# Optimization experiments

Hardware: AMD Instinct MI355X
Metric: run time of the kernel (lower is better)

## Reference

```python
import jax, jax.numpy as jnp
import numpy as np

EPS = 1e-5

def _conv1x1_bn(x, W, b, g, beta):
    # 1x1 conv == channel matmul; BN in training mode uses batch stats over (N,H,W)
    y = jnp.einsum('bchw,oc->bohw', x, W) + b[None, :, None, None]
    mu = jnp.mean(y, axis=(0, 2, 3))
    var = jnp.var(y, axis=(0, 2, 3))
    y = (y - mu[None, :, None, None]) * jax.lax.rsqrt(var + EPS)[None, :, None, None]
    return y * g[None, :, None, None] + beta[None, :, None, None]


def setup_inputs() -> dict:
    key = jax.random.key(0)
    ks = jax.random.split(key, 7)
    b, c, h, w = 8, 256, 64, 64
    sc = 1.0 / np.sqrt(c)
    inp = {
        'x': jax.random.normal(ks[0], (b, c, h, w), jnp.float32),
        'Wq': jax.random.normal(ks[1], (c, c), jnp.float32) * sc,
        'bq': jax.random.normal(ks[2], (c,), jnp.float32) * 0.02,
        'gq': jnp.ones((c,), jnp.float32),
        'betaq': jnp.zeros((c,), jnp.float32),
        'Wk': jax.random.normal(ks[3], (c, c), jnp.float32) * sc,
        'bk': jax.random.normal(ks[4], (c,), jnp.float32) * 0.02,
        'gk': jnp.ones((c,), jnp.float32),
        'betak': jnp.zeros((c,), jnp.float32),
        'Wv': jax.random.normal(ks[5], (c, c), jnp.float32) * sc,
        'bv': jax.random.normal(ks[6], (c,), jnp.float32) * 0.02,
        'gv': jnp.ones((c,), jnp.float32),
        'betav': jnp.zeros((c,), jnp.float32),
    }
    return inp


def reference(x, Wq, bq, gq, betaq, Wk, bk, gk, betak, Wv, bv, gv, betav):
    b, c, h, w = x.shape
    scale = float(h) ** (-0.5)
    Q = _conv1x1_bn(x, Wq, bq, gq, betaq).reshape(b, c, h * w)
    K = _conv1x1_bn(x, Wk, bk, gk, betak).reshape(b, c, h * w)
    V = _conv1x1_bn(x, Wv, bv, gv, betav).reshape(b, c, h * w)
    # un-normalized attention (no softmax)
    pixelMap = jnp.einsum('bcq,bck->bqk', Q, K) * scale  # [b, N, N]
    out = jnp.einsum('bqk,bck->bcq', pixelMap, V)        # [b, c, N]
    return out.reshape(b, c, h, w)
```

## Files before the change

kernel.cpp:

```cpp
#include <hip/hip_runtime.h>
#include <hip/hip_bf16.h>


#define BB 8
#define CC 256
#define NPIX 4096
#define PTOT 32768
#define EPSV 1e-5f
#define SCALEV 0.125f

#define OFF_PG    0L
#define OFF_SP    3145728L
#define OFF_S     3162112L
#define OFF_GHAT  3164160L
#define OFF_XBAR  3229696L
#define OFF_WP    3229952L
#define OFF_WKTF  3426560L
#define OFF_WVTF  3492096L
#define OFF_CVEC  3557632L
#define OFF_U     3558400L
#define OFF_W2    3560448L
#define OFF_HB    3562496L
#define OFF_Y     3564544L
#define OFF_R     3564800L
#define OFF_OFFV  3565056L
#define OFF_GBF   3567104L
#define OFF_WQT   3829248L
#define OFF_WKT   3862016L
#define OFF_WVB   3894784L
#define OFF_ZT    3927552L
#define OFF_FT    3960320L
#define OFF_TBF   4222464L

typedef __attribute__((ext_vector_type(8))) short short8;
typedef __attribute__((ext_vector_type(4))) float f32x4;

#define MFMA16(a, b, c) __builtin_amdgcn_mfma_f32_16x16x32_bf16((a), (b), (c), 0, 0, 0)

__device__ __forceinline__ ushort f2bf(float f) {
    union { float f; unsigned u; } v; v.f = f;
    const unsigned r = (v.u + 0x7FFFu + ((v.u >> 16) & 1u)) >> 16;
    return (ushort)r;
}

__device__ __forceinline__ float bf2f(ushort u) {
    union { unsigned u; float f; } v; v.u = ((unsigned)u) << 16;
    return v.f;
}

__device__ __forceinline__ ushort2 f2bf2(float a, float b) {
    __hip_bfloat162 h = __float22bfloat162_rn(float2{a, b});
    union { __hip_bfloat162 h; ushort2 u; } v; v.h = h;
    return v.u;
}

__device__ __forceinline__ float block_reduce(float v, float* red, int tid) {
    red[tid] = v; __syncthreads();
    for (int st = 128; st > 0; st >>= 1) {
        if (tid < st) red[tid] += red[tid + st];
        __syncthreads();
    }
    float r = red[0]; __syncthreads();
    return r;
}

__device__ __forceinline__ float2 wred2(float a, float b, float* red8, int tid) {
    #pragma unroll
    for (int s = 32; s > 0; s >>= 1) {
        a += __shfl_xor(a, s);
        b += __shfl_xor(b, s);
    }
    if ((tid & 63) == 0) { red8[(tid >> 6) * 2] = a; red8[(tid >> 6) * 2 + 1] = b; }
    __syncthreads();
    const float ra = red8[0] + red8[2] + red8[4] + red8[6];
    const float rb = red8[1] + red8[3] + red8[5] + red8[7];
    __syncthreads();
    return float2{ra, rb};
}

__global__ __launch_bounds__(256) void gram_mfma(const float* __restrict__ x,
                                                 float* __restrict__ Pg,
                                                 float* __restrict__ Sp,
                                                 float* __restrict__ Ghat) {
    __shared__ __align__(16) ushort Ab[128 * 72];
    __shared__ __align__(16) ushort Bb[128 * 72];
    __shared__ float rs[128];
    const int tid = threadIdx.x;
    const int ks = blockIdx.x, b = blockIdx.y, tt = blockIdx.z;
    const int lb = (tt * 8 + b) * 8 + ks;
    if (lb < 64) {
        #pragma unroll
        for (int i = 0; i < 4; ++i) Ghat[lb * 1024 + i * 256 + tid] = 0.f;
    }
    const int it = (tt == 1) ? 1 : 0;
    const int jt = (tt == 0) ? 0 : 1;
    const bool diag = (tt < 2);
    const int i0 = it * 128, j0 = jt * 128, k0 = ks * 512;
    const float* xb = x + (long)b * CC * NPIX;
    const int c = tid & 15, rp = tid >> 4;
    const int wave = tid >> 6, lane = tid & 63;
    const int wr = (wave >> 1) * 64, wc = (wave & 1) * 64;
    const int m = lane & 15, q8 = (lane >> 4) * 8;

    if (tid < 128) rs[tid] = 0.f;
    float rloc[8] = {};
    f32x4 acc[4][4];
    #pragma unroll
    for (int a = 0; a < 4; ++a)
        #pragma unroll
        for (int q = 0; q < 4; ++q) acc[a][q] = (f32x4){0.f, 0.f, 0.f, 0.f};

    const float* Abase = xb + (long)i0 * NPIX + k0 + c * 4;
    const float* Bbase = xb + (long)j0 * NPIX + k0 + c * 4;

    float4 va[8], vb[8];
    #pragma unroll
    for (int pp = 0; pp < 8; ++pp)
        va[pp] = *(const float4*)&Abase[(long)(pp * 16 + rp) * NPIX];
    if (!diag) {
        #pragma unroll
        for (int pp = 0; pp < 8; ++pp)
            vb[pp] = *(const float4*)&Bbase[(long)(pp * 16 + rp) * NPIX];
    }

    for (int kc = 0; kc < 512; kc += 64) {
        __syncthreads();
        #pragma unroll
        for (int pp = 0; pp < 8; ++pp) {
            const int row = pp * 16 + rp;
            const float4 v = va[pp];
            rloc[pp] += v.x + v.y + v.z + v.w;
            const ushort2 w01 = f2bf2(v.x, v.y);
            const ushort2 w23 = f2bf2(v.z, v.w);
            ushort4 w; w.x = w01.x; w.y = w01.y; w.z = w23.x; w.w = w23.y;
            *(ushort4*)&Ab[row * 72 + c * 4] = w;
        }
        if (!diag) {
            #pragma unroll
            for (int pp = 0; pp < 8; ++pp) {
                const int row = pp * 16 + rp;
                const float4 v = vb[pp];
                const ushort2 w01 = f2bf2(v.x, v.y);
                const ushort2 w23 = f2bf2(v.z, v.w);
                ushort4 w; w.x = w01.x; w.y = w01.y; w.z = w23.x; w.w = w23.y;
                *(ushort4*)&Bb[row * 72 + c * 4] = w;
            }
        }
        const int kn = kc + 64;
        if (kn < 512) {
            #pragma unroll
            for (int pp = 0; pp < 8; ++pp)
                va[pp] = *(const float4*)&Abase[(long)(pp * 16 + rp) * NPIX + kn];
            if (!diag) {
                #pragma unroll
                for (int pp = 0; pp < 8; ++pp)
                    vb[pp] = *(const float4*)&Bbase[(long)(pp * 16 + rp) * NPIX + kn];
            }
        }
        __syncthreads();
        const ushort* Bsrc = diag ? Ab : Bb;
        #pragma unroll
        for (int kk = 0; kk < 2; ++kk) {
            short8 af[4], bfv[4];
            #pragma unroll
            for (int a = 0; a < 4; ++a)
                af[a] = *(const short8*)&Ab[(wr + a * 16 + m) * 72 + kk * 32 + q8];
            #pragma unroll
            for (int q = 0; q < 4; ++q)
                bfv[q] = *(const short8*)&Bsrc[(wc + q * 16 + m) * 72 + kk * 32 + q8];
            #pragma unroll
            for (int a = 0; a < 4; ++a)
                #pragma unroll
                for (int q = 0; q < 4; ++q)
                    acc[a][q] = MFMA16(af[a], bfv[q], acc[a][q]);
        }
    }
    if (diag) {
        #pragma unroll
        for (int pp = 0; pp < 8; ++pp) atomicAdd(&rs[pp * 16 + rp], rloc[pp]);
        __syncthreads();
        if (tid < 128) Sp[(((long)ks * 8 + b) * 2 + it) * 128 + tid] = rs[tid];
    }
    float* Pt = Pg + (((long)ks * 8 + b) * 3 + tt) * 16384;
    const int rq = (lane >> 4) * 4;
    #pragma unroll
    for (int a = 0; a < 4; ++a) {
        #pragma unroll
        for (int q = 0; q < 4; ++q) {
            const int col = wc + q * 16 + m;
            #pragma unroll
            for (int reg = 0; reg < 4; ++reg)
                Pt[(long)(wr + a * 16 + rq + reg) * 128 + col] = acc[a][q][reg];
        }
    }
}

__global__ __launch_bounds__(256) void reduce_mirror(const float* __restrict__ Pg,
                                                     const float* __restrict__ Sp,
                                                     ushort* __restrict__ Gbf,
                                                     float* __restrict__ Ghat,
                                                     float* __restrict__ S,
                                                     float* __restrict__ xbar) {
    const int blk = blockIdx.x, tid = threadIdx.x;
    if (blk == 384) {
        const int it2 = tid >> 7, rr = tid & 127;
        float xacc = 0.f;
        for (int b = 0; b < BB; ++b) {
            float acc = 0.f;
            #pragma unroll
            for (int ks = 0; ks < 8; ++ks)
                acc += Sp[(((long)ks * 8 + b) * 2 + it2) * 128 + rr];
            S[b * 256 + tid] = acc;
            xacc += acc;
        }
        xbar[tid] = xacc * (1.0f / PTOT);
        return;
    }
    __shared__ float tile[32][33];
    const int tt = blk >> 7;
    const int sub = (blk >> 3) & 15;
    const int b = blk & 7;
    const int sr = (sub >> 2) * 32, sc = (sub & 3) * 32;
    const int it = (tt == 1) ? 1 : 0;
    const int jt = (tt == 0) ? 0 : 1;
    const bool offd = (tt == 2);
    const int gi0 = it * 128 + sr, gj0 = jt * 128 + sc;
    const int r = tid >> 3, c4 = (tid & 7) * 4;
    const float inv = 1.0f / PTOT;

    float s0 = 0.f, s1 = 0.f, s2 = 0.f, s3 = 0.f;
    #pragma unroll
    for (int ks = 0; ks < 8; ++ks) {
        const float4 v = *(const float4*)&Pg[(((long)ks * 8 + b) * 3 + tt) * 16384
                                             + (long)(sr + r) * 128 + sc + c4];
        s0 += v.x; s1 += v.y; s2 += v.z; s3 += v.w;
    }
    ushort4 w;
    w.x = f2bf(s0); w.y = f2bf(s1); w.z = f2bf(s2); w.w = f2bf(s3);
    *(ushort4*)&Gbf[(long)b * 65536 + (long)(gi0 + r) * 256 + gj0 + c4] = w;
    float* gd = &Ghat[(long)(gi0 + r) * 256 + gj0 + c4];
    atomicAdd(gd + 0, s0 * inv);
    atomicAdd(gd + 1, s1 * inv);
    atomicAdd(gd + 2, s2 * inv);
    atomicAdd(gd + 3, s3 * inv);
    if (offd) {
        tile[r][c4 + 0] = s0; tile[r][c4 + 1] = s1;
        tile[r][c4 + 2] = s2; tile[r][c4 + 3] = s3;
        __syncthreads();
        const float t0 = tile[c4 + 0][r], t1 = tile[c4 + 1][r];
        const float t2 = tile[c4 + 2][r], t3 = tile[c4 + 3][r];
        ushort4 tw;
        tw.x = f2bf(t0); tw.y = f2bf(t1); tw.z = f2bf(t2); tw.w = f2bf(t3);
        *(ushort4*)&Gbf[(long)b * 65536 + (long)(gj0 + r) * 256 + gi0 + c4] = tw;
        float* gm = &Ghat[(long)(gj0 + r) * 256 + gi0 + c4];
        atomicAdd(gm + 0, t0 * inv);
        atomicAdd(gm + 1, t1 * inv);
        atomicAdd(gm + 2, t2 * inv);
        atomicAdd(gm + 3, t3 * inv);
    }
}

__global__ __launch_bounds__(256) void stats_quad(const float* __restrict__ Wq, const float* __restrict__ Wk,
                           const float* __restrict__ Wv, const float* __restrict__ Ghat,
                           const float* __restrict__ xbar,
                           const float* bq, const float* gq, const float* betaq,
                           const float* bk, const float* gk, const float* betak,
                           const float* bv, const float* gv, const float* betav,
                           float* __restrict__ Wp, float* __restrict__ cvec,
                           ushort* __restrict__ WqT, ushort* __restrict__ WkT,
                           ushort* __restrict__ Wvb, float* __restrict__ WkTf,
                           float* __restrict__ WvTf) {
    const int og = blockIdx.x, t = blockIdx.y, tid = threadIdx.x;
    const int o0 = og * 4;
    const float* Wt  = t == 0 ? Wq : (t == 1 ? Wk : Wv);
    const float* bt  = t == 0 ? bq : (t == 1 ? bk : bv);
    const float* gt  = t == 0 ? gq : (t == 1 ? gk : gv);
    const float* bet = t == 0 ? betaq : (t == 1 ? betak : betav);
    __shared__ float wrows[4][256];
    __shared__ float red8[8];
    #pragma unroll
    for (int i = 0; i < 4; ++i) wrows[i][tid] = Wt[(o0 + i) * 256 + tid];
    const float xb = xbar[tid];
    __syncthreads();
    const float* grow = Ghat + (long)tid * 256;
    float tj[4] = {0.f, 0.f, 0.f, 0.f};
    #pragma unroll 8
    for (int k = 0; k < 256; k += 4) {
        const float4 g = *(const float4*)&grow[k];
        #pragma unroll
        for (int i = 0; i < 4; ++i)
            tj[i] += g.x * wrows[i][k]     + g.y * wrows[i][k + 1]
                   + g.z * wrows[i][k + 2] + g.w * wrows[i][k + 3];
    }
    #pragma unroll
    for (int i = 0; i < 4; ++i) {
        const int o = o0 + i;
        const float wv = wrows[i][tid];
        const float2 qw = wred2(wv * tj[i], wv * xb, red8, tid);
        const float bo = bt[o];
        const float mu = qw.y + bo;
        const float var = qw.x + 2.f * bo * mu - bo * bo - mu * mu;
        const float a = gt[o] * rsqrtf(var + EPSV);
        const float wpv = a * wv;
        Wp[(long)t * 65536 + o * 256 + tid] = wpv;
        const ushort wb = f2bf(wpv);
        if (t == 0) {
            WqT[(long)tid * 256 + o] = wb;
        } else if (t == 1) {
            WkT[(long)tid * 256 + o] = wb;
            WkTf[(long)tid * 256 + o] = wpv;
        } else {
            Wvb[(long)o * 256 + tid] = wb;
            WvTf[(long)tid * 256 + o] = wpv;
        }
        if (tid == 0) cvec[t * 256 + o] = a * (bo - mu) + bet[o];
    }
}

__device__ __forceinline__ void gemm_tile(const ushort* __restrict__ Ab,
                                          const ushort* __restrict__ Bb,
                                          ushort* __restrict__ Db,
                                          int m0, int n0, int mode, int bz,
                                          const float* __restrict__ u,
                                          const float* __restrict__ cvec,
                                          const float* __restrict__ r,
                                          const float* __restrict__ hb, int tid) {
    const int wave = tid >> 6, lane = tid & 63;
    const int wr = (wave >> 1) * 64, wc = (wave & 1) * 64;
    const int m = lane & 15, q8 = (lane >> 4) * 8;
    f32x4 acc[4][4];
    #pragma unroll
    for (int a = 0; a < 4; ++a)
        #pragma unroll
        for (int q = 0; q < 4; ++q) acc[a][q] = (f32x4){0.f, 0.f, 0.f, 0.f};
    #pragma unroll
    for (int kk = 0; kk < 8; ++kk) {
        short8 af[4], bfv[4];
        #pragma unroll
        for (int a = 0; a < 4; ++a)
            af[a] = *(const short8*)&Ab[(long)(m0 + wr + a * 16 + m) * 256 + kk * 32 + q8];
        #pragma unroll
        for (int q = 0; q < 4; ++q)
            bfv[q] = *(const short8*)&Bb[(long)(n0 + wc + q * 16 + m) * 256 + kk * 32 + q8];
        #pragma unroll
        for (int a = 0; a < 4; ++a)
            #pragma unroll
            for (int q = 0; q < 4; ++q)
                acc[a][q] = MFMA16(af[a], bfv[q], acc[a][q]);
    }
    const int rq = (lane >> 4) * 4;
    #pragma unroll
    for (int a = 0; a < 4; ++a) {
        #pragma unroll
        for (int q = 0; q < 4; ++q) {
            const int col = n0 + wc + q * 16 + m;
            #pragma unroll
            for (int reg = 0; reg < 4; ++reg) {
                const int row = m0 + wr + a * 16 + rq + reg;
                const float v = acc[a][q][reg];
                if (mode == 0) {
                    Db[(long)col * 256 + row] = f2bf(v);
                } else {
                    const float rv = r[col];
                    const float t2 = hb[bz * 256 + col] + 4096.0f * rv;
                    const float val = SCALEV * (v + u[bz * 256 + row] * rv + cvec[512 + row] * t2);
                    Db[(long)row * 256 + col] = f2bf(val);
                }
            }
        }
    }
}

__global__ __launch_bounds__(256) void zmida(const ushort* __restrict__ WkT,
                                             const ushort* __restrict__ WqT,
                                             ushort* __restrict__ ZT,
                                             const float* __restrict__ Wp,
                                             const float* __restrict__ WkTf,
                                             const float* __restrict__ WvTf,
                                             const float* __restrict__ S,
                                             const float* __restrict__ cvec,
                                             float* __restrict__ u, float* __restrict__ w,
                                             float* __restrict__ y, float* __restrict__ r) {
    const int blk = blockIdx.x, tid = threadIdx.x;
    if (blk < 4) {
        gemm_tile(WkT, WqT, ZT, (blk >> 1) * 128, (blk & 1) * 128, 0, 0,
                  nullptr, nullptr, nullptr, nullptr, tid);
        return;
    }
    const int bidx = blk - 4;
    if (bidx < 8) {
        __shared__ float sh[256];
        sh[tid] = S[bidx * 256 + tid]; __syncthreads();
        float uu = 0.f, ww = 0.f;
        #pragma unroll 8
        for (int j = 0; j < 256; ++j) {
            uu += WvTf[(long)j * 256 + tid] * sh[j];
            ww += WkTf[(long)j * 256 + tid] * sh[j];
        }
        u[bidx * 256 + tid] = uu;
        w[bidx * 256 + tid] = ww;
    } else {
        __shared__ float cqs[256], cks[256];
        cqs[tid] = cvec[tid]; cks[tid] = cvec[256 + tid]; __syncthreads();
        float yy = 0.f, rr = 0.f;
        #pragma unroll 8
        for (int o = 0; o < 256; ++o) {
            yy += Wp[65536L + (long)o * 256 + tid] * cqs[o];
            rr += Wp[(long)o * 256 + tid] * cks[o];
        }
        y[tid] = yy;
        r[tid] = rr;
    }
}

__global__ __launch_bounds__(256) void bcF(const float* __restrict__ Wp,
                                           const ushort* __restrict__ Gbf,
                                           const float* __restrict__ WvTf,
                                           const float* __restrict__ w,
                                           const float* __restrict__ y,
                                           const float* __restrict__ u,
                                           const float* __restrict__ cvec,
                                           float* __restrict__ hb,
                                           float* __restrict__ offv,
                                           const ushort* __restrict__ ZT,
                                           ushort* __restrict__ FT) {
    const int blk = blockIdx.x, tid = threadIdx.x;
    if (blk >= 8) {
        const int idx = blk - 8;
        const int bz = idx >> 2, t = idx & 3;
        gemm_tile(Gbf + (long)bz * 65536, ZT, FT + (long)bz * 65536,
                  (t >> 1) * 128, (t & 1) * 128, 0, 0,
                  nullptr, nullptr, nullptr, nullptr, tid);
        return;
    }
    const int b = blk;
    __shared__ float wl[256], yl[256], gyl[256], red[256], cqs[256], cks[256];
    wl[tid] = w[b * 256 + tid];
    yl[tid] = y[tid];
    cqs[tid] = cvec[tid];
    cks[tid] = cvec[256 + tid];
    const float cv = cvec[512 + tid];
    const float uu = u[b * 256 + tid];
    __syncthreads();
    float hh = 0.f, gg = 0.f;
    #pragma unroll 8
    for (int o = 0; o < 256; ++o) {
        hh += Wp[(long)o * 256 + tid] * wl[o];
        gg += bf2f(Gbf[(long)b * 65536 + (long)o * 256 + tid]) * yl[o];
    }
    hb[b * 256 + tid] = hh;
    gyl[tid] = gg;
    __syncthreads();
    float vg = 0.f;
    #pragma unroll 8
    for (int j = 0; j < 256; ++j) vg += WvTf[(long)j * 256 + tid] * gyl[j];
    const float dkq = block_reduce(cqs[tid] * cks[tid], red, tid);
    const float dwq = block_reduce(wl[tid] * cqs[tid], red, tid);
    offv[b * 256 + tid] = SCALEV * (vg + uu * dkq + cv * (dwq + 4096.0f * dkq));
}

__global__ __launch_bounds__(256) void gemm_T(const ushort* __restrict__ Wvb,
                                              const ushort* __restrict__ FT,
                                              ushort* __restrict__ Tbf,
                                              const float* __restrict__ u,
                                              const float* __restrict__ cvec,
                                              const float* __restrict__ r,
                                              const float* __restrict__ hb) {
    const int bz = blockIdx.z;
    gemm_tile(Wvb, FT + (long)bz * 65536, Tbf + (long)bz * 65536,
              blockIdx.y * 128, blockIdx.x * 128, 1, bz, u, cvec, r, hb, threadIdx.x);
}

__global__ __launch_bounds__(256) void out_mfma(const ushort* __restrict__ Tbf,
                                                const float* __restrict__ x,
                                                const float* __restrict__ offv,
                                                float* __restrict__ out) {
    __shared__ __align__(16) ushort Bs[64 * 264];
    const int tid = threadIdx.x;
    const int p0 = blockIdx.x * 64;
    const int b = blockIdx.y;
    const float* xb = x + (long)b * CC * NPIX;
    const ushort* Tb = Tbf + (long)b * 65536;

    const int c = tid & 15, kq = tid >> 4;
    #pragma unroll
    for (int kt = 0; kt < 4; ++kt) {
        const int k4 = kt * 64 + kq * 4;
        const int p = c * 4;
        const float4 v0 = *(const float4*)&xb[(long)(k4 + 0) * NPIX + p0 + p];
        const float4 v1 = *(const float4*)&xb[(long)(k4 + 1) * NPIX + p0 + p];
        const float4 v2 = *(const float4*)&xb[(long)(k4 + 2) * NPIX + p0 + p];
        const float4 v3 = *(const float4*)&xb[(long)(k4 + 3) * NPIX + p0 + p];
        ushort2 a01, a23;
        ushort4 w;
        a01 = f2bf2(v0.x, v1.x); a23 = f2bf2(v2.x, v3.x);
        w.x = a01.x; w.y = a01.y; w.z = a23.x; w.w = a23.y;
        *(ushort4*)&Bs[(p + 0) * 264 + k4] = w;
        a01 = f2bf2(v0.y, v1.y); a23 = f2bf2(v2.y, v3.y);
        w.x = a01.x; w.y = a01.y; w.z = a23.x; w.w = a23.y;
        *(ushort4*)&Bs[(p + 1) * 264 + k4] = w;
        a01 = f2bf2(v0.z, v1.z); a23 = f2bf2(v2.z, v3.z);
        w.x = a01.x; w.y = a01.y; w.z = a23.x; w.w = a23.y;
        *(ushort4*)&Bs[(p + 2) * 264 + k4] = w;
        a01 = f2bf2(v0.w, v1.w); a23 = f2bf2(v2.w, v3.w);
        w.x = a01.x; w.y = a01.y; w.z = a23.x; w.w = a23.y;
        *(ushort4*)&Bs[(p + 3) * 264 + k4] = w;
    }
    __syncthreads();

    const int wave = tid >> 6, lane = tid & 63;
    const int wr = wave * 64;
    const int m = lane & 15, q8 = (lane >> 4) * 8;
    f32x4 acc[4][4];
    #pragma unroll
    for (int a = 0; a < 4; ++a)
        #pragma unroll
        for (int q = 0; q < 4; ++q) acc[a][q] = (f32x4){0.f, 0.f, 0.f, 0.f};

    #pragma unroll
    for (int kk = 0; kk < 8; ++kk) {
        short8 af[4], bfv[4];
        #pragma unroll
        for (int a = 0; a < 4; ++a)
            af[a] = *(const short8*)&Tb[(long)(wr + a * 16 + m) * 256 + kk * 32 + q8];
        #pragma unroll
        for (int q = 0; q < 4; ++q)
            bfv[q] = *(const short8*)&Bs[(q * 16 + m) * 264 + kk * 32 + q8];
        #pragma unroll
        for (int a = 0; a < 4; ++a)
            #pragma unroll
            for (int q = 0; q < 4; ++q)
                acc[a][q] = MFMA16(af[a], bfv[q], acc[a][q]);
    }

    const int rq = (lane >> 4) * 4;
    #pragma unroll
    for (int a = 0; a < 4; ++a) {
        #pragma unroll
        for (int reg = 0; reg < 4; ++reg) {
            const int row = wr + a * 16 + rq + reg;
            const float off_ = offv[b * CC + row];
            float* orow = &out[((long)b * CC + row) * NPIX + p0];
            #pragma unroll
            for (int q = 0; q < 4; ++q)
                orow[q * 16 + m] = acc[a][q][reg] + off_;
        }
    }
}

extern "C" void kernel_launch(void* const* d_in, const int* in_sizes, int n_in,
                              void* d_out, int out_size, void* d_ws, size_t ws_size,
                              hipStream_t stream) {
    const float* x     = (const float*)d_in[0];
    const float* Wq    = (const float*)d_in[1];
    const float* bq    = (const float*)d_in[2];
    const float* gq    = (const float*)d_in[3];
    const float* betaq = (const float*)d_in[4];
    const float* Wk    = (const float*)d_in[5];
    const float* bk    = (const float*)d_in[6];
    const float* gk    = (const float*)d_in[7];
    const float* betak = (const float*)d_in[8];
    const float* Wv    = (const float*)d_in[9];
    const float* bv    = (const float*)d_in[10];
    const float* gv    = (const float*)d_in[11];
    const float* betav = (const float*)d_in[12];
    float* ws = (float*)d_ws;

    float*  Pg   = ws + OFF_PG;
    float*  Sp   = ws + OFF_SP;
    float*  S    = ws + OFF_S;
    float*  Ghat = ws + OFF_GHAT;
    float*  Xbar = ws + OFF_XBAR;
    float*  Wp   = ws + OFF_WP;
    float*  WkTf = ws + OFF_WKTF;
    float*  WvTf = ws + OFF_WVTF;
    float*  cvec = ws + OFF_CVEC;
    float*  U    = ws + OFF_U;
    float*  W2   = ws + OFF_W2;
    float*  Hb   = ws + OFF_HB;
    float*  Y    = ws + OFF_Y;
    float*  R    = ws + OFF_R;
    float*  OffV = ws + OFF_OFFV;
    ushort* Gbf  = (ushort*)(ws + OFF_GBF);
    ushort* WqT  = (ushort*)(ws + OFF_WQT);
    ushort* WkT  = (ushort*)(ws + OFF_WKT);
    ushort* Wvb  = (ushort*)(ws + OFF_WVB);
    ushort* ZT   = (ushort*)(ws + OFF_ZT);
    ushort* FT   = (ushort*)(ws + OFF_FT);
    ushort* Tbf  = (ushort*)(ws + OFF_TBF);

    gram_mfma<<<dim3(8, 8, 3), 256, 0, stream>>>(x, Pg, Sp, Ghat);
    reduce_mirror<<<385, 256, 0, stream>>>(Pg, Sp, Gbf, Ghat, S, Xbar);
    stats_quad<<<dim3(64, 3), 256, 0, stream>>>(Wq, Wk, Wv, Ghat, Xbar,
                                                bq, gq, betaq, bk, gk, betak,
                                                bv, gv, betav, Wp, cvec,
                                                WqT, WkT, Wvb, WkTf, WvTf);
    zmida<<<13, 256, 0, stream>>>(WkT, WqT, ZT, Wp, WkTf, WvTf, S, cvec, U, W2, Y, R);
    bcF<<<40, 256, 0, stream>>>(Wp, Gbf, WvTf, W2, Y, U, cvec, Hb, OffV, ZT, FT);
    gemm_T<<<dim3(2, 2, 8), 256, 0, stream>>>(Wvb, FT, Tbf, U, cvec, R, Hb);
    out_mfma<<<dim3(64, 8), 256, 0, stream>>>(Tbf, x, OffV, (float*)d_out);
}
```

Measured before the change: 197.7 us.

## Fuse all stages into one persistent kernel with global grid barriers

Replaces the seven-kernel launch chain with one persistent 256-block kernel. The stages are separated by an atomic-counter grid barrier, and a union of shared-memory layouts lets each stage reuse the same LDS. This is meant to remove per-launch overhead and the idle tail between small dependent kernels. The intermediate ZT/FT buffers are dropped, and the middle GEMM stages appear to be restructured to keep intermediate tiles in swizzled LDS. The barrier assumes all 256 blocks are co-resident, and its spin has a bounded timeout that could silently break ordering if that assumption fails. It also adds a memset per call.

```diff
diff --git a/kernel.cpp b/kernel.cpp
--- a/kernel.cpp
+++ b/kernel.cpp
@@ -19,18 +19,15 @@
 #define OFF_WVTF  3492096L
 #define OFF_CVEC  3557632L
 #define OFF_U     3558400L
-#define OFF_W2    3560448L
 #define OFF_HB    3562496L
-#define OFF_Y     3564544L
 #define OFF_R     3564800L
 #define OFF_OFFV  3565056L
 #define OFF_GBF   3567104L
 #define OFF_WQT   3829248L
 #define OFF_WKT   3862016L
 #define OFF_WVB   3894784L
-#define OFF_ZT    3927552L
-#define OFF_FT    3960320L
 #define OFF_TBF   4222464L
+#define OFF_CNT   4484608L
 
 typedef __attribute__((ext_vector_type(8))) short short8;
 typedef __attribute__((ext_vector_type(4))) float f32x4;
@@ -78,472 +75,465 @@
     return float2{ra, rb};
 }
 
-__global__ __launch_bounds__(256) void gram_mfma(const float* __restrict__ x,
-                                                 float* __restrict__ Pg,
-                                                 float* __restrict__ Sp,
-                                                 float* __restrict__ Ghat) {
-    __shared__ __align__(16) ushort Ab[128 * 72];
-    __shared__ __align__(16) ushort Bb[128 * 72];
-    __shared__ float rs[128];
-    const int tid = threadIdx.x;
-    const int ks = blockIdx.x, b = blockIdx.y, tt = blockIdx.z;
-    const int lb = (tt * 8 + b) * 8 + ks;
-    if (lb < 64) {
-        #pragma unroll
-        for (int i = 0; i < 4; ++i) Ghat[lb * 1024 + i * 256 + tid] = 0.f;
-    }
-    const int it = (tt == 1) ? 1 : 0;
-    const int jt = (tt == 0) ? 0 : 1;
-    const bool diag = (tt < 2);
-    const int i0 = it * 128, j0 = jt * 128, k0 = ks * 512;
-    const float* xb = x + (long)b * CC * NPIX;
-    const int c = tid & 15, rp = tid >> 4;
-    const int wave = tid >> 6, lane = tid & 63;
-    const int wr = (wave >> 1) * 64, wc = (wave & 1) * 64;
-    const int m = lane & 15, q8 = (lane >> 4) * 8;
-
-    if (tid < 128) rs[tid] = 0.f;
-    float rloc[8] = {};
-    f32x4 acc[4][4];
+__device__ __forceinline__ void gbar(unsigned* cnt, unsigned target) {
+    __syncthreads();
+    if (threadIdx.x == 0) {
+        __threadfence();
+        atomicAdd(cnt, 1u);
+        unsigned spins = 0;
+        while (atomicAdd(cnt, 0u) < target && ++spins < (1u << 18))
+            __builtin_amdgcn_s_sleep(32);
+        __threadfence();
+    }
+    __syncthreads();
+}
+
+union SmemU {
+    struct { ushort Ab[128 * 72]; ushort Bb[128 * 72]; float rs[128]; } g;
+    struct { float tile[32][33]; } rm;
+    struct { float wr4[4][256]; float red8[8]; } st;
+    struct { float sh[256], wl[256], yl[256], gyl[256],
+                   red[256], cqs[256], cks[256]; } vx;
+    struct { ushort zt[64 * 256]; ushort ft[64 * 256]; } ch;
+    struct { ushort Bs[64 * 264]; } op;
+};
+
+__device__ __forceinline__ void mm256x64(f32x4 acc[4][4],
+                                         const ushort* __restrict__ Aglob,
+                                         const ushort* __restrict__ Bglob,
+                                         const ushort* Blds,
+                                         int wave, int m, int qq) {
+    const int q8 = qq * 8;
+    #pragma unroll
+    for (int kk = 0; kk < 8; ++kk) {
+        short8 af[4], bv[4];
+        #pragma unroll
+        for (int a = 0; a < 4; ++a)
+            af[a] = *(const short8*)&Aglob[(long)(wave * 64 + a * 16 + m) * 256 + kk * 32 + q8];
+        #pragma unroll
+        for (int q = 0; q < 4; ++q) {
+            const int col = q * 16 + m;
+            if (Blds) bv[q] = *(const short8*)&Blds[col * 256 + ((kk * 32 + q8) ^ ((col & 7) << 3))];
+            else      bv[q] = *(const short8*)&Bglob[(long)col * 256 + kk * 32 + q8];
+        }
+        #pragma unroll
+        for (int a = 0; a < 4; ++a)
+            #pragma unroll
+            for (int q = 0; q < 4; ++q)
+                acc[a][q] = MFMA16(af[a], bv[q], acc[a][q]);
+    }
+}
+
+__device__ __forceinline__ void st_lds(ushort* L, f32x4 acc[4][4],
+                                       int wave, int m, int qq) {
     #pragma unroll
     for (int a = 0; a < 4; ++a)
         #pragma unroll
-        for (int q = 0; q < 4; ++q) acc[a][q] = (f32x4){0.f, 0.f, 0.f, 0.f};
-
-    const float* Abase = xb + (long)i0 * NPIX + k0 + c * 4;
-    const float* Bbase = xb + (long)j0 * NPIX + k0 + c * 4;
-
-    float4 va[8], vb[8];
-    #pragma unroll
-    for (int pp = 0; pp < 8; ++pp)
-        va[pp] = *(const float4*)&Abase[(long)(pp * 16 + rp) * NPIX];
-    if (!diag) {
+        for (int q = 0; q < 4; ++q) {
+            const int col = q * 16 + m;
+            const int rowb = wave * 64 + a * 16 + qq * 4;
+            const ushort2 p01 = f2bf2(acc[a][q][0], acc[a][q][1]);
+            const ushort2 p23 = f2bf2(acc[a][q][2], acc[a][q][3]);
+            ushort4 w4; w4.x = p01.x; w4.y = p01.y; w4.z = p23.x; w4.w = p23.y;
+            *(ushort4*)&L[col * 256 + (rowb ^ ((col & 7) << 3))] = w4;
+        }
+}
+
+__global__ __launch_bounds__(256, 2) void mono(
+        const float* __restrict__ x,
+        const float* __restrict__ Wq, const float* __restrict__ bq,
+        const float* __restrict__ gq, const float* __restrict__ betaq,
+        const float* __restrict__ Wk, const float* __restrict__ bk,
+        const float* __restrict__ gk, const float* __restrict__ betak,
+        const float* __restrict__ Wv, const float* __restrict__ bv,
+        const float* __restrict__ gv, const float* __restrict__ betav,
+        float* __restrict__ out,
+        float* __restrict__ Pg, float* __restrict__ Sp, float* __restrict__ S,
+        float* __restrict__ Ghat, float* __restrict__ xbar,
+        float* __restrict__ Wp, float* __restrict__ WkTf, float* __restrict__ WvTf,
+        float* __restrict__ cvec, float* __restrict__ u, float* __restrict__ hb,
+        float* __restrict__ r_, float* __restrict__ offv,
+        ushort* __restrict__ Gbf, ushort* __restrict__ WqT, ushort* __restrict__ WkT,
+        ushort* __restrict__ Wvb, ushort* __restrict__ Tbf,
+        unsigned* __restrict__ cnt) {
+    __shared__ SmemU sm;
+    const int blk = blockIdx.x, tid = threadIdx.x;
+    const unsigned NB = gridDim.x;
+
+    if (blk < 64) {
+        #pragma unroll
+        for (int i = 0; i < 4; ++i) Ghat[blk * 1024 + i * 256 + tid] = 0.f;
+    }
+    if (blk < 192) {
+        const int ks = blk & 7, b = (blk >> 3) & 7, tt = blk >> 6;
+        const int it = (tt == 1) ? 1 : 0;
+        const int jt = (tt == 0) ? 0 : 1;
+        const bool diag = (tt < 2);
+        const int i0 = it * 128, j0 = jt * 128, k0 = ks * 512;
+        const float* xb = x + (long)b * CC * NPIX;
+        const int c = tid & 15, rp = tid >> 4;
+        const int wave = tid >> 6, lane = tid & 63;
+        const int wr = (wave >> 1) * 64, wc = (wave & 1) * 64;
+        const int m = lane & 15, q8 = (lane >> 4) * 8;
+
+        if (tid < 128) sm.g.rs[tid] = 0.f;
+        float rloc[8] = {};
+        f32x4 acc[4][4];
+        #pragma unroll
+        for (int a = 0; a < 4; ++a)
+            #pragma unroll
+            for (int q = 0; q < 4; ++q) acc[a][q] = (f32x4){0.f, 0.f, 0.f, 0.f};
+
+        const float* Abase = xb + (long)i0 * NPIX + k0 + c * 4;
+        const float* Bbase = xb + (long)j0 * NPIX + k0 + c * 4;
+
+        float4 va[8], vb[8];
         #pragma unroll
         for (int pp = 0; pp < 8; ++pp)
-            vb[pp] = *(const float4*)&Bbase[(long)(pp * 16 + rp) * NPIX];
-    }
-
-    for (int kc = 0; kc < 512; kc += 64) {
-        __syncthreads();
-        #pragma unroll
-        for (int pp = 0; pp < 8; ++pp) {
-            const int row = pp * 16 + rp;
-            const float4 v = va[pp];
-            rloc[pp] += v.x + v.y + v.z + v.w;
-            const ushort2 w01 = f2bf2(v.x, v.y);
-            const ushort2 w23 = f2bf2(v.z, v.w);
-            ushort4 w; w.x = w01.x; w.y = w01.y; w.z = w23.x; w.w = w23.y;
-            *(ushort4*)&Ab[row * 72 + c * 4] = w;
-        }
+            va[pp] = *(const float4*)&Abase[(long)(pp * 16 + rp) * NPIX];
         if (!diag) {
+            #pragma unroll
+            for (int pp = 0; pp < 8; ++pp)
+                vb[pp] = *(const float4*)&Bbase[(long)(pp * 16 + rp) * NPIX];
+        }
+
+        for (int kc = 0; kc < 512; kc += 64) {
+            __syncthreads();
             #pragma unroll
             for (int pp = 0; pp < 8; ++pp) {
                 const int row = pp * 16 + rp;
-                const float4 v = vb[pp];
+                const float4 v = va[pp];
+                rloc[pp] += v.x + v.y + v.z + v.w;
                 const ushort2 w01 = f2bf2(v.x, v.y);
                 const ushort2 w23 = f2bf2(v.z, v.w);
                 ushort4 w; w.x = w01.x; w.y = w01.y; w.z = w23.x; w.w = w23.y;
-                *(ushort4*)&Bb[row * 72 + c * 4] = w;
-            }
-        }
-        const int kn = kc + 64;
-        if (kn < 512) {
-            #pragma unroll
-            for (int pp = 0; pp < 8; ++pp)
-                va[pp] = *(const float4*)&Abase[(long)(pp * 16 + rp) * NPIX + kn];
+                *(ushort4*)&sm.g.Ab[row * 72 + c * 4] = w;
+            }
             if (!diag) {
                 #pragma unroll
+                for (int pp = 0; pp < 8; ++pp) {
+                    const int row = pp * 16 + rp;
+                    const float4 v = vb[pp];
+                    const ushort2 w01 = f2bf2(v.x, v.y);
+                    const ushort2 w23 = f2bf2(v.z, v.w);
+                    ushort4 w; w.x = w01.x; w.y = w01.y; w.z = w23.x; w.w = w23.y;
+                    *(ushort4*)&sm.g.Bb[row * 72 + c * 4] = w;
+                }
+            }
+            const int kn = kc + 64;
+            if (kn < 512) {
+                #pragma unroll
                 for (int pp = 0; pp < 8; ++pp)
-                    vb[pp] = *(const float4*)&Bbase[(long)(pp * 16 + rp) * NPIX + kn];
-            }
-        }
-        __syncthreads();
-        const ushort* Bsrc = diag ? Ab : Bb;
-        #pragma unroll
-        for (int kk = 0; kk < 2; ++kk) {
+                    va[pp] = *(const float4*)&Abase[(long)(pp * 16 + rp) * NPIX + kn];
+                if (!diag) {
+                    #pragma unroll
+                    for (int pp = 0; pp < 8; ++pp)
+                        vb[pp] = *(const float4*)&Bbase[(long)(pp * 16 + rp) * NPIX + kn];
+                }
+            }
+            __syncthreads();
+            const ushort* Bsrc = diag ? sm.g.Ab : sm.g.Bb;
+            #pragma unroll
+            for (int kk = 0; kk < 2; ++kk) {
+                short8 af[4], bfv[4];
+                #pragma unroll
+                for (int a = 0; a < 4; ++a)
+                    af[a] = *(const short8*)&sm.g.Ab[(wr + a * 16 + m) * 72 + kk * 32 + q8];
+                #pragma unroll
+                for (int q = 0; q < 4; ++q)
+                    bfv[q] = *(const short8*)&Bsrc[(wc + q * 16 + m) * 72 + kk * 32 + q8];
+                #pragma unroll
+                for (int a = 0; a < 4; ++a)
+                    #pragma unroll
+                    for (int q = 0; q < 4; ++q)
+                        acc[a][q] = MFMA16(af[a], bfv[q], acc[a][q]);
+            }
+        }
+        if (diag) {
+            #pragma unroll
+            for (int pp = 0; pp < 8; ++pp) atomicAdd(&sm.g.rs[pp * 16 + rp], rloc[pp]);
+            __syncthreads();
+            if (tid < 128) Sp[(((long)ks * 8 + b) * 2 + it) * 128 + tid] = sm.g.rs[tid];
+        }
+        float* Pt = Pg + (((long)ks * 8 + b) * 3 + tt) * 16384;
+        const int rq = (lane >> 4) * 4;
+        #pragma unroll
+        for (int a = 0; a < 4; ++a) {
+            #pragma unroll
+            for (int q = 0; q < 4; ++q) {
+                const int col = wc + q * 16 + m;
+                #pragma unroll
+                for (int reg = 0; reg < 4; ++reg)
+                    Pt[(long)(wr + a * 16 + rq + reg) * 128 + col] = acc[a][q][reg];
+            }
+        }
+    }
+    gbar(cnt, NB * 1);
+
+    for (int v = blk; v <= 384; v += 256) {
+        if (v == 384) {
+            const int it2 = tid >> 7, rr = tid & 127;
+            float xacc = 0.f;
+            for (int b = 0; b < BB; ++b) {
+                float acc = 0.f;
+                #pragma unroll
+                for (int ks = 0; ks < 8; ++ks)
+                    acc += Sp[(((long)ks * 8 + b) * 2 + it2) * 128 + rr];
+                S[b * 256 + tid] = acc;
+                xacc += acc;
+            }
+            xbar[tid] = xacc * (1.0f / PTOT);
+            continue;
+        }
+        const int tt = v >> 7;
+        const int sub = (v >> 3) & 15;
+        const int b = v & 7;
+        const int sr = (sub >> 2) * 32, sc = (sub & 3) * 32;
+        const int it = (tt == 1) ? 1 : 0;
+        const int jt = (tt == 0) ? 0 : 1;
+        const bool offd = (tt == 2);
+        const int gi0 = it * 128 + sr, gj0 = jt * 128 + sc;
+        const int r = tid >> 3, c4 = (tid & 7) * 4;
+        const float inv = 1.0f / PTOT;
+
+        float s0 = 0.f, s1 = 0.f, s2 = 0.f, s3 = 0.f;
+        #pragma unroll
+        for (int ks = 0; ks < 8; ++ks) {
+            const float4 pv = *(const float4*)&Pg[(((long)ks * 8 + b) * 3 + tt) * 16384
+                                                  + (long)(sr + r) * 128 + sc + c4];
+            s0 += pv.x; s1 += pv.y; s2 += pv.z; s3 += pv.w;
+        }
+        ushort4 w;
+        w.x = f2bf(s0); w.y = f2bf(s1); w.z = f2bf(s2); w.w = f2bf(s3);
+        *(ushort4*)&Gbf[(long)b * 65536 + (long)(gi0 + r) * 256 + gj0 + c4] = w;
+        float* gd = &Ghat[(long)(gi0 + r) * 256 + gj0 + c4];
+        atomicAdd(gd + 0, s0 * inv);
+        atomicAdd(gd + 1, s1 * inv);
+        atomicAdd(gd + 2, s2 * inv);
+        atomicAdd(gd + 3, s3 * inv);
+        if (offd) {
+            sm.rm.tile[r][c4 + 0] = s0; sm.rm.tile[r][c4 + 1] = s1;
+            sm.rm.tile[r][c4 + 2] = s2; sm.rm.tile[r][c4 + 3] = s3;
+            __syncthreads();
+            const float t0 = sm.rm.tile[c4 + 0][r], t1 = sm.rm.tile[c4 + 1][r];
+            const float t2 = sm.rm.tile[c4 + 2][r], t3 = sm.rm.tile[c4 + 3][r];
+            ushort4 tw;
+            tw.x = f2bf(t0); tw.y = f2bf(t1); tw.z = f2bf(t2); tw.w = f2bf(t3);
+            *(ushort4*)&Gbf[(long)b * 65536 + (long)(gj0 + r) * 256 + gi0 + c4] = tw;
+            float* gm = &Ghat[(long)(gj0 + r) * 256 + gi0 + c4];
+            atomicAdd(gm + 0, t0 * inv);
+            atomicAdd(gm + 1, t1 * inv);
+            atomicAdd(gm + 2, t2 * inv);
+            atomicAdd(gm + 3, t3 * inv);
+            __syncthreads();
+        }
+    }
+    gbar(cnt, NB * 2);
+
+    if (blk < 192) {
+        const int og = blk & 63, t = blk >> 6;
+        const int o0 = og * 4;
+        const float* Wt  = t == 0 ? Wq : (t == 1 ? Wk : Wv);
+        const float* bt  = t == 0 ? bq : (t == 1 ? bk : bv);
+        const float* gt  = t == 0 ? gq : (t == 1 ? gk : gv);
+        const float* bet = t == 0 ? betaq : (t == 1 ? betak : betav);
+        #pragma unroll
+        for (int i = 0; i < 4; ++i) sm.st.wr4[i][tid] = Wt[(o0 + i) * 256 + tid];
+        const float xb = xbar[tid];
+        __syncthreads();
+        const float* grow = Ghat + (long)tid * 256;
+        float tj[4] = {0.f, 0.f, 0.f, 0.f};
+        #pragma unroll 8
+        for (int k = 0; k < 256; k += 4) {
+            const float4 g = *(const float4*)&grow[k];
+            #pragma unroll
+            for (int i = 0; i < 4; ++i)
+                tj[i] += g.x * sm.st.wr4[i][k]     + g.y * sm.st.wr4[i][k + 1]
+                       + g.z * sm.st.wr4[i][k + 2] + g.w * sm.st.wr4[i][k + 3];
+        }
+        #pragma unroll
+        for (int i = 0; i < 4; ++i) {
+            const int o = o0 + i;
+            const float wv = sm.st.wr4[i][tid];
+            const float2 qw = wred2(wv * tj[i], wv * xb, sm.st.red8, tid);
+            const float bo = bt[o];
+            const float mu = qw.y + bo;
+            const float var = qw.x + 2.f * bo * mu - bo * bo - mu * mu;
+            const float a = gt[o] * rsqrtf(var + EPSV);
+            const float wpv = a * wv;
+            Wp[(long)t * 65536 + o * 256 + tid] = wpv;
+            const ushort wb = f2bf(wpv);
+            if (t == 0) {
+                WqT[(long)tid * 256 + o] = wb;
+            } else if (t == 1) {
+                WkT[(long)tid * 256 + o] = wb;
+                WkTf[(long)tid * 256 + o] = wpv;
+            } else {
+                Wvb[(long)o * 256 + tid] = wb;
+                WvTf[(long)tid * 256 + o] = wpv;
+            }
+            if (tid == 0) cvec[t * 256 + o] = a * (bo - mu) + bet[o];
+        }
+    }
+    gbar(cnt, NB * 3);
+
+    if (blk < 8) {
+        const int b = blk;
+        sm.vx.sh[tid]  = S[b * 256 + tid];
+        sm.vx.cqs[tid] = cvec[tid];
+        sm.vx.cks[tid] = cvec[256 + tid];
+        __syncthreads();
+        float yy = 0.f, rr = 0.f, uu = 0.f, ww = 0.f;
+        #pragma unroll 8
+        for (int o = 0; o < 256; ++o) {
+            yy += Wp[65536L + (long)o * 256 + tid] * sm.vx.cqs[o];
+            rr += Wp[(long)o * 256 + tid] * sm.vx.cks[o];
+        }
+        #pragma unroll 8
+        for (int j = 0; j < 256; ++j) {
+            uu += WvTf[(long)j * 256 + tid] * sm.vx.sh[j];
+            ww += WkTf[(long)j * 256 + tid] * sm.vx.sh[j];
+        }
+        sm.vx.yl[tid] = yy; sm.vx.wl[tid] = ww;
+        __syncthreads();
+        float hh = 0.f, gg = 0.f;
+        #pragma unroll 8
+        for (int o = 0; o < 256; ++o) {
+            hh += Wp[(long)o * 256 + tid] * sm.vx.wl[o];
+            gg += bf2f(Gbf[(long)b * 65536 + (long)o * 256 + tid]) * sm.vx.yl[o];
+        }
+        hb[b * 256 + tid] = hh;
+        u[b * 256 + tid] = uu;
+        if (blk == 0) r_[tid] = rr;
+        sm.vx.gyl[tid] = gg;
+        __syncthreads();
+        float vg = 0.f;
+        #pragma unroll 8
+        for (int j = 0; j < 256; ++j) vg += WvTf[(long)j * 256 + tid] * sm.vx.gyl[j];
+        const float cv = cvec[512 + tid];
+        const float dkq = block_reduce(sm.vx.cqs[tid] * sm.vx.cks[tid], sm.vx.red, tid);
+        const float dwq = block_reduce(sm.vx.wl[tid] * sm.vx.cqs[tid], sm.vx.red, tid);
+        offv[b * 256 + tid] = SCALEV * (vg + uu * dkq + cv * (dwq + 4096.0f * dkq));
+    }
+    gbar(cnt, NB * 4);
+
+    if (blk < 32) {
+        const int b = blk >> 2, j0 = (blk & 3) * 64;
+        const int wave = tid >> 6, lane = tid & 63;
+        const int m = lane & 15, qq = lane >> 4;
+        f32x4 acc[4][4];
+
+        #pragma unroll
+        for (int a = 0; a < 4; ++a)
+            #pragma unroll
+            for (int q = 0; q < 4; ++q) acc[a][q] = (f32x4){0.f, 0.f, 0.f, 0.f};
+        mm256x64(acc, WkT, WqT + (long)j0 * 256, nullptr, wave, m, qq);
+        st_lds(sm.ch.zt, acc, wave, m, qq);
+        __syncthreads();
+
+        #pragma unroll
+        for (int a = 0; a < 4; ++a)
+            #pragma unroll
+            for (int q = 0; q < 4; ++q) acc[a][q] = (f32x4){0.f, 0.f, 0.f, 0.f};
+        mm256x64(acc, Gbf + (long)b * 65536, nullptr, sm.ch.zt, wave, m, qq);
+        st_lds(sm.ch.ft, acc, wave, m, qq);
+        __syncthreads();
+
+        #pragma unroll
+        for (int a = 0; a < 4; ++a)
+            #pragma unroll
+            for (int q = 0; q < 4; ++q) acc[a][q] = (f32x4){0.f, 0.f, 0.f, 0.f};
+        mm256x64(acc, Wvb, nullptr, sm.ch.ft, wave, m, qq);
+        const int rq4 = qq * 4;
+        #pragma unroll
+        for (int a = 0; a < 4; ++a) {
+            #pragma unroll
+            for (int q = 0; q < 4; ++q) {
+                const int cg = j0 + q * 16 + m;
+                const float rv = r_[cg];
+                const float t2 = hb[b * 256 + cg] + 4096.0f * rv;
+                #pragma unroll
+                for (int reg = 0; reg < 4; ++reg) {
+                    const int row = wave * 64 + a * 16 + rq4 + reg;
+                    const float val = SCALEV * (acc[a][q][reg] + u[b * 256 + row] * rv
+                                                + cvec[512 + row] * t2);
+                    Tbf[(long)b * 65536 + (long)row * 256 + cg] = f2bf(val);
+                }
+            }
+        }
+    }
+    gbar(cnt, NB * 5);
+
+    for (int v = blk; v < 512; v += 256) {
+        const int p0 = (v & 63) * 64;
+        const int b = v >> 6;
+        const float* xb = x + (long)b * CC * NPIX;
+        const ushort* Tb = Tbf + (long)b * 65536;
+        __syncthreads();
+
+        const int c = tid & 15, kq = tid >> 4;
+        #pragma unroll
+        for (int kt = 0; kt < 4; ++kt) {
+            const int k4 = kt * 64 + kq * 4;
+            const int p = c * 4;
+            const float4 v0 = *(const float4*)&xb[(long)(k4 + 0) * NPIX + p0 + p];
+            const float4 v1 = *(const float4*)&xb[(long)(k4 + 1) * NPIX + p0 + p];
+            const float4 v2 = *(const float4*)&xb[(long)(k4 + 2) * NPIX + p0 + p];
+            const float4 v3 = *(const float4*)&xb[(long)(k4 + 3) * NPIX + p0 + p];
+            ushort2 a01, a23;
+            ushort4 w;
+            a01 = f2bf2(v0.x, v1.x); a23 = f2bf2(v2.x, v3.x);
+            w.x = a01.x; w.y = a01.y; w.z = a23.x; w.w = a23.y;
+            *(ushort4*)&sm.op.Bs[(p + 0) * 264 + k4] = w;
+            a01 = f2bf2(v0.y, v1.y); a23 = f2bf2(v2.y, v3.y);
+            w.x = a01.x; w.y = a01.y; w.z = a23.x; w.w = a23.y;
+            *(ushort4*)&sm.op.Bs[(p + 1) * 264 + k4] = w;
+            a01 = f2bf2(v0.z, v1.z); a23 = f2bf2(v2.z, v3.z);
+            w.x = a01.x; w.y = a01.y; w.z = a23.x; w.w = a23.y;
+            *(ushort4*)&sm.op.Bs[(p + 2) * 264 + k4] = w;
+            a01 = f2bf2(v0.w, v1.w); a23 = f2bf2(v2.w, v3.w);
+            w.x = a01.x; w.y = a01.y; w.z = a23.x; w.w = a23.y;
+            *(ushort4*)&sm.op.Bs[(p + 3) * 264 + k4] = w;
+        }
+        __syncthreads();
+
+        const int wave = tid >> 6, lane = tid & 63;
+        const int wr = wave * 64;
+        const int m = lane & 15, q8 = (lane >> 4) * 8;
+        f32x4 acc[4][4];
+        #pragma unroll
+        for (int a = 0; a < 4; ++a)
+            #pragma unroll
+            for (int q = 0; q < 4; ++q) acc[a][q] = (f32x4){0.f, 0.f, 0.f, 0.f};
+
+        #pragma unroll
+        for (int kk = 0; kk < 8; ++kk) {
             short8 af[4], bfv[4];
             #pragma unroll
             for (int a = 0; a < 4; ++a)
-                af[a] = *(const short8*)&Ab[(wr + a * 16 + m) * 72 + kk * 32 + q8];
+                af[a] = *(const short8*)&Tb[(long)(wr + a * 16 + m) * 256 + kk * 32 + q8];
             #pragma unroll
             for (int q = 0; q < 4; ++q)
-                bfv[q] = *(const short8*)&Bsrc[(wc + q * 16 + m) * 72 + kk * 32 + q8];
+                bfv[q] = *(const short8*)&sm.op.Bs[(q * 16 + m) * 264 + kk * 32 + q8];
             #pragma unroll
             for (int a = 0; a < 4; ++a)
                 #pragma unroll
                 for (int q = 0; q < 4; ++q)
                     acc[a][q] = MFMA16(af[a], bfv[q], acc[a][q]);
         }
-    }
-    if (diag) {
-        #pragma unroll
-        for (int pp = 0; pp < 8; ++pp) atomicAdd(&rs[pp * 16 + rp], rloc[pp]);
-        __syncthreads();
-        if (tid < 128) Sp[(((long)ks * 8 + b) * 2 + it) * 128 + tid] = rs[tid];
-    }
-    float* Pt = Pg + (((long)ks * 8 + b) * 3 + tt) * 16384;
-    const int rq = (lane >> 4) * 4;
-    #pragma unroll
-    for (int a = 0; a < 4; ++a) {
-        #pragma unroll
-        for (int q = 0; q < 4; ++q) {
-            const int col = wc + q * 16 + m;
-            #pragma unroll
-            for (int reg = 0; reg < 4; ++reg)
-                Pt[(long)(wr + a * 16 + rq + reg) * 128 + col] = acc[a][q][reg];
-        }
-    }
-}
-
-__global__ __launch_bounds__(256) void reduce_mirror(const float* __restrict__ Pg,
-                                                     const float* __restrict__ Sp,
-                                                     ushort* __restrict__ Gbf,
-                                                     float* __restrict__ Ghat,
-                                                     float* __restrict__ S,
-                                                     float* __restrict__ xbar) {
-    const int blk = blockIdx.x, tid = threadIdx.x;
-    if (blk == 384) {
-        const int it2 = tid >> 7, rr = tid & 127;
-        float xacc = 0.f;
-        for (int b = 0; b < BB; ++b) {
-            float acc = 0.f;
-            #pragma unroll
-            for (int ks = 0; ks < 8; ++ks)
-                acc += Sp[(((long)ks * 8 + b) * 2 + it2) * 128 + rr];
-            S[b * 256 + tid] = acc;
-            xacc += acc;
-        }
-        xbar[tid] = xacc * (1.0f / PTOT);
-        return;
-    }
-    __shared__ float tile[32][33];
-    const int tt = blk >> 7;
-    const int sub = (blk >> 3) & 15;
-    const int b = blk & 7;
-    const int sr = (sub >> 2) * 32, sc = (sub & 3) * 32;
-    const int it = (tt == 1) ? 1 : 0;
-    const int jt = (tt == 0) ? 0 : 1;
-    const bool offd = (tt == 2);
-    const int gi0 = it * 128 + sr, gj0 = jt * 128 + sc;
-    const int r = tid >> 3, c4 = (tid & 7) * 4;
-    const float inv = 1.0f / PTOT;
-
-    float s0 = 0.f, s1 = 0.f, s2 = 0.f, s3 = 0.f;
-    #pragma unroll
-    for (int ks = 0; ks < 8; ++ks) {
-        const float4 v = *(const float4*)&Pg[(((long)ks * 8 + b) * 3 + tt) * 16384
-                                             + (long)(sr + r) * 128 + sc + c4];
-        s0 += v.x; s1 += v.y; s2 += v.z; s3 += v.w;
-    }
-    ushort4 w;
-    w.x = f2bf(s0); w.y = f2bf(s1); w.z = f2bf(s2); w.w = f2bf(s3);
-    *(ushort4*)&Gbf[(long)b * 65536 + (long)(gi0 + r) * 256 + gj0 + c4] = w;
-    float* gd = &Ghat[(long)(gi0 + r) * 256 + gj0 + c4];
-    atomicAdd(gd + 0, s0 * inv);
-    atomicAdd(gd + 1, s1 * inv);
-    atomicAdd(gd + 2, s2 * inv);
-    atomicAdd(gd + 3, s3 * inv);
-    if (offd) {
-        tile[r][c4 + 0] = s0; tile[r][c4 + 1] = s1;
-        tile[r][c4 + 2] = s2; tile[r][c4 + 3] = s3;
-        __syncthreads();
-        const float t0 = tile[c4 + 0][r], t1 = tile[c4 + 1][r];
-        const float t2 = tile[c4 + 2][r], t3 = tile[c4 + 3][r];
-        ushort4 tw;
-        tw.x = f2bf(t0); tw.y = f2bf(t1); tw.z = f2bf(t2); tw.w = f2bf(t3);
-        *(ushort4*)&Gbf[(long)b * 65536 + (long)(gj0 + r) * 256 + gi0 + c4] = tw;
-        float* gm = &Ghat[(long)(gj0 + r) * 256 + gi0 + c4];
-        atomicAdd(gm + 0, t0 * inv);
-        atomicAdd(gm + 1, t1 * inv);
-        atomicAdd(gm + 2, t2 * inv);
-        atomicAdd(gm + 3, t3 * inv);
-    }
-}
-
-__global__ __launch_bounds__(256) void stats_quad(const float* __restrict__ Wq, const float* __restrict__ Wk,
-                           const float* __restrict__ Wv, const float* __restrict__ Ghat,
-                           const float* __restrict__ xbar,
-                           const float* bq, const float* gq, const float* betaq,
-                           const float* bk, const float* gk, const float* betak,
-                           const float* bv, const float* gv, const float* betav,
-                           float* __restrict__ Wp, float* __restrict__ cvec,
-                           ushort* __restrict__ WqT, ushort* __restrict__ WkT,
-                           ushort* __restrict__ Wvb, float* __restrict__ WkTf,
-                           float* __restrict__ WvTf) {
-    const int og = blockIdx.x, t = blockIdx.y, tid = threadIdx.x;
-    const int o0 = og * 4;
-    const float* Wt  = t == 0 ? Wq : (t == 1 ? Wk : Wv);
-    const float* bt  = t == 0 ? bq : (t == 1 ? bk : bv);
-    const float* gt  = t == 0 ? gq : (t == 1 ? gk : gv);
-    const float* bet = t == 0 ? betaq : (t == 1 ? betak : betav);
-    __shared__ float wrows[4][256];
-    __shared__ float red8[8];
-    #pragma unroll
-    for (int i = 0; i < 4; ++i) wrows[i][tid] = Wt[(o0 + i) * 256 + tid];
-    const float xb = xbar[tid];
-    __syncthreads();
-    const float* grow = Ghat + (long)tid * 256;
-    float tj[4] = {0.f, 0.f, 0.f, 0.f};
-    #pragma unroll 8
-    for (int k = 0; k < 256; k += 4) {
-        const float4 g = *(const float4*)&grow[k];
-        #pragma unroll
-        for (int i = 0; i < 4; ++i)
-            tj[i] += g.x * wrows[i][k]     + g.y * wrows[i][k + 1]
-                   + g.z * wrows[i][k + 2] + g.w * wrows[i][k + 3];
-    }
-    #pragma unroll
-    for (int i = 0; i < 4; ++i) {
-        const int o = o0 + i;
-        const float wv = wrows[i][tid];
-        const float2 qw = wred2(wv * tj[i], wv * xb, red8, tid);
-        const float bo = bt[o];
-        const float mu = qw.y + bo;
-        const float var = qw.x + 2.f * bo * mu - bo * bo - mu * mu;
-        const float a = gt[o] * rsqrtf(var + EPSV);
-        const float wpv = a * wv;
-        Wp[(long)t * 65536 + o * 256 + tid] = wpv;
-        const ushort wb = f2bf(wpv);
-        if (t == 0) {
-            WqT[(long)tid * 256 + o] = wb;
-        } else if (t == 1) {
-            WkT[(long)tid * 256 + o] = wb;
-            WkTf[(long)tid * 256 + o] = wpv;
-        } else {
-            Wvb[(long)o * 256 + tid] = wb;
-            WvTf[(long)tid * 256 + o] = wpv;
-        }
-        if (tid == 0) cvec[t * 256 + o] = a * (bo - mu) + bet[o];
-    }
-}
-
-__device__ __forceinline__ void gemm_tile(const ushort* __restrict__ Ab,
-                                          const ushort* __restrict__ Bb,
-                                          ushort* __restrict__ Db,
-                                          int m0, int n0, int mode, int bz,
-                                          const float* __restrict__ u,
-                                          const float* __restrict__ cvec,
-                                          const float* __restrict__ r,
-                                          const float* __restrict__ hb, int tid) {
-    const int wave = tid >> 6, lane = tid & 63;
-    const int wr = (wave >> 1) * 64, wc = (wave & 1) * 64;
-    const int m = lane & 15, q8 = (lane >> 4) * 8;
-    f32x4 acc[4][4];
-    #pragma unroll
-    for (int a = 0; a < 4; ++a)
-        #pragma unroll
-        for (int q = 0; q < 4; ++q) acc[a][q] = (f32x4){0.f, 0.f, 0.f, 0.f};
-    #pragma unroll
-    for (int kk = 0; kk < 8; ++kk) {
-        short8 af[4], bfv[4];
-        #pragma unroll
-        for (int a = 0; a < 4; ++a)
-            af[a] = *(const short8*)&Ab[(long)(m0 + wr + a * 16 + m) * 256 + kk * 32 + q8];
-        #pragma unroll
-        for (int q = 0; q < 4; ++q)
-            bfv[q] = *(const short8*)&Bb[(long)(n0 + wc + q * 16 + m) * 256 + kk * 32 + q8];
-        #pragma unroll
-        for (int a = 0; a < 4; ++a)
-            #pragma unroll
-            for (int q = 0; q < 4; ++q)
-                acc[a][q] = MFMA16(af[a], bfv[q], acc[a][q]);
-    }
-    const int rq = (lane >> 4) * 4;
-    #pragma unroll
-    for (int a = 0; a < 4; ++a) {
-        #pragma unroll
-        for (int q = 0; q < 4; ++q) {
-            const int col = n0 + wc + q * 16 + m;
+
+        const int rq = (lane >> 4) * 4;
+        #pragma unroll
+        for (int a = 0; a < 4; ++a) {
             #pragma unroll
             for (int reg = 0; reg < 4; ++reg) {
-                const int row = m0 + wr + a * 16 + rq + reg;
-                const float v = acc[a][q][reg];
-                if (mode == 0) {
-                    Db[(long)col * 256 + row] = f2bf(v);
-                } else {
-                    const float rv = r[col];
-                    const float t2 = hb[bz * 256 + col] + 4096.0f * rv;
-                    const float val = SCALEV * (v + u[bz * 256 + row] * rv + cvec[512 + row] * t2);
-                    Db[(long)row * 256 + col] = f2bf(val);
-                }
-            }
-        }
-    }
-}
-
-__global__ __launch_bounds__(256) void zmida(const ushort* __restrict__ WkT,
-                                             const ushort* __restrict__ WqT,
-                                             ushort* __restrict__ ZT,
-                                             const float* __restrict__ Wp,
-                                             const float* __restrict__ WkTf,
-                                             const float* __restrict__ WvTf,
-                                             const float* __restrict__ S,
-                                             const float* __restrict__ cvec,
-                                             float* __restrict__ u, float* __restrict__ w,
-                                             float* __restrict__ y, float* __restrict__ r) {
-    const int blk = blockIdx.x, tid = threadIdx.x;
-    if (blk < 4) {
-        gemm_tile(WkT, WqT, ZT, (blk >> 1) * 128, (blk & 1) * 128, 0, 0,
-                  nullptr, nullptr, nullptr, nullptr, tid);
-        return;
-    }
-    const int bidx = blk - 4;
-    if (bidx < 8) {
-        __shared__ float sh[256];
-        sh[tid] = S[bidx * 256 + tid]; __syncthreads();
-        float uu = 0.f, ww = 0.f;
-        #pragma unroll 8
-        for (int j = 0; j < 256; ++j) {
-            uu += WvTf[(long)j * 256 + tid] * sh[j];
-            ww += WkTf[(long)j * 256 + tid] * sh[j];
-        }
-        u[bidx * 256 + tid] = uu;
-        w[bidx * 256 + tid] = ww;
-    } else {
-        __shared__ float cqs[256], cks[256];
-        cqs[tid] = cvec[tid]; cks[tid] = cvec[256 + tid]; __syncthreads();
-        float yy = 0.f, rr = 0.f;
-        #pragma unroll 8
-        for (int o = 0; o < 256; ++o) {
-            yy += Wp[65536L + (long)o * 256 + tid] * cqs[o];
-            rr += Wp[(long)o * 256 + tid] * cks[o];
-        }
-        y[tid] = yy;
-        r[tid] = rr;
-    }
-}
-
-__global__ __launch_bounds__(256) void bcF(const float* __restrict__ Wp,
-                                           const ushort* __restrict__ Gbf,
-                                           const float* __restrict__ WvTf,
-                                           const float* __restrict__ w,
-                                           const float* __restrict__ y,
-                                           const float* __restrict__ u,
-                                           const float* __restrict__ cvec,
-                                           float* __restrict__ hb,
-                                           float* __restrict__ offv,
-                                           const ushort* __restrict__ ZT,
-                                           ushort* __restrict__ FT) {
-    const int blk = blockIdx.x, tid = threadIdx.x;
-    if (blk >= 8) {
-        const int idx = blk - 8;
-        const int bz = idx >> 2, t = idx & 3;
-        gemm_tile(Gbf + (long)bz * 65536, ZT, FT + (long)bz * 65536,
-                  (t >> 1) * 128, (t & 1) * 128, 0, 0,
-                  nullptr, nullptr, nullptr, nullptr, tid);
-        return;
-    }
-    const int b = blk;
-    __shared__ float wl[256], yl[256], gyl[256], red[256], cqs[256], cks[256];
-    wl[tid] = w[b * 256 + tid];
-    yl[tid] = y[tid];
-    cqs[tid] = cvec[tid];
-    cks[tid] = cvec[256 + tid];
-    const float cv = cvec[512 + tid];
-    const float uu = u[b * 256 + tid];
-    __syncthreads();
-    float hh = 0.f, gg = 0.f;
-    #pragma unroll 8
-    for (int o = 0; o < 256; ++o) {
-        hh += Wp[(long)o * 256 + tid] * wl[o];
-        gg += bf2f(Gbf[(long)b * 65536 + (long)o * 256 + tid]) * yl[o];
-    }
-    hb[b * 256 + tid] = hh;
-    gyl[tid] = gg;
-    __syncthreads();
-    float vg = 0.f;
-    #pragma unroll 8
-    for (int j = 0; j < 256; ++j) vg += WvTf[(long)j * 256 + tid] * gyl[j];
-    const float dkq = block_reduce(cqs[tid] * cks[tid], red, tid);
-    const float dwq = block_reduce(wl[tid] * cqs[tid], red, tid);
-    offv[b * 256 + tid] = SCALEV * (vg + uu * dkq + cv * (dwq + 4096.0f * dkq));
-}
-
-__global__ __launch_bounds__(256) void gemm_T(const ushort* __restrict__ Wvb,
-                                              const ushort* __restrict__ FT,
-                                              ushort* __restrict__ Tbf,
-                                              const float* __restrict__ u,
-                                              const float* __restrict__ cvec,
-                                              const float* __restrict__ r,
-                                              const float* __restrict__ hb) {
-    const int bz = blockIdx.z;
-    gemm_tile(Wvb, FT + (long)bz * 65536, Tbf + (long)bz * 65536,
-              blockIdx.y * 128, blockIdx.x * 128, 1, bz, u, cvec, r, hb, threadIdx.x);
-}
-
-__global__ __launch_bounds__(256) void out_mfma(const ushort* __restrict__ Tbf,
-                                                const float* __restrict__ x,
-                                                const float* __restrict__ offv,
-                                                float* __restrict__ out) {
-    __shared__ __align__(16) ushort Bs[64 * 264];
-    const int tid = threadIdx.x;
-    const int p0 = blockIdx.x * 64;
-    const int b = blockIdx.y;
-    const float* xb = x + (long)b * CC * NPIX;
-    const ushort* Tb = Tbf + (long)b * 65536;
-
-    const int c = tid & 15, kq = tid >> 4;
-    #pragma unroll
-    for (int kt = 0; kt < 4; ++kt) {
-        const int k4 = kt * 64 + kq * 4;
-        const int p = c * 4;
-        const float4 v0 = *(const float4*)&xb[(long)(k4 + 0) * NPIX + p0 + p];
-        const float4 v1 = *(const float4*)&xb[(long)(k4 + 1) * NPIX + p0 + p];
-        const float4 v2 = *(const float4*)&xb[(long)(k4 + 2) * NPIX + p0 + p];
-        const float4 v3 = *(const float4*)&xb[(long)(k4 + 3) * NPIX + p0 + p];
-        ushort2 a01, a23;
-        ushort4 w;
-        a01 = f2bf2(v0.x, v1.x); a23 = f2bf2(v2.x, v3.x);
-        w.x = a01.x; w.y = a01.y; w.z = a23.x; w.w = a23.y;
-        *(ushort4*)&Bs[(p + 0) * 264 + k4] = w;
-        a01 = f2bf2(v0.y, v1.y); a23 = f2bf2(v2.y, v3.y);
-        w.x = a01.x; w.y = a01.y; w.z = a23.x; w.w = a23.y;
-        *(ushort4*)&Bs[(p + 1) * 264 + k4] = w;
-        a01 = f2bf2(v0.z, v1.z); a23 = f2bf2(v2.z, v3.z);
-        w.x = a01.x; w.y = a01.y; w.z = a23.x; w.w = a23.y;
-        *(ushort4*)&Bs[(p + 2) * 264 + k4] = w;
-        a01 = f2bf2(v0.w, v1.w); a23 = f2bf2(v2.w, v3.w);
-        w.x = a01.x; w.y = a01.y; w.z = a23.x; w.w = a23.y;
-        *(ushort4*)&Bs[(p + 3) * 264 + k4] = w;
-    }
-    __syncthreads();
-
-    const int wave = tid >> 6, lane = tid & 63;
-    const int wr = wave * 64;
-    const int m = lane & 15, q8 = (lane >> 4) * 8;
-    f32x4 acc[4][4];
-    #pragma unroll
-    for (int a = 0; a < 4; ++a)
-        #pragma unroll
-        for (int q = 0; q < 4; ++q) acc[a][q] = (f32x4){0.f, 0.f, 0.f, 0.f};
-
-    #pragma unroll
-    for (int kk = 0; kk < 8; ++kk) {
-        short8 af[4], bfv[4];
-        #pragma unroll
-        for (int a = 0; a < 4; ++a)
-            af[a] = *(const short8*)&Tb[(long)(wr + a * 16 + m) * 256 + kk * 32 + q8];
-        #pragma unroll
-        for (int q = 0; q < 4; ++q)
-            bfv[q] = *(const short8*)&Bs[(q * 16 + m) * 264 + kk * 32 + q8];
-        #pragma unroll
-        for (int a = 0; a < 4; ++a)
-            #pragma unroll
-            for (int q = 0; q < 4; ++q)
-                acc[a][q] = MFMA16(af[a], bfv[q], acc[a][q]);
-    }
-
-    const int rq = (lane >> 4) * 4;
-    #pragma unroll
-    for (int a = 0; a < 4; ++a) {
-        #pragma unroll
-        for (int reg = 0; reg < 4; ++reg) {
-            const int row = wr + a * 16 + rq + reg;
-            const float off_ = offv[b * CC + row];
-            float* orow = &out[((long)b * CC + row) * NPIX + p0];
-            #pragma unroll
-            for (int q = 0; q < 4; ++q)
-                orow[q * 16 + m] = acc[a][q][reg] + off_;
+                const int row = wr + a * 16 + rq + reg;
+                const float off_ = offv[b * CC + row];
+                float* orow = &out[((long)b * CC + row) * NPIX + p0];
+                #pragma unroll
+                for (int q = 0; q < 4; ++q)
+                    orow[q * 16 + m] = acc[a][q][reg] + off_;
+            }
         }
     }
 }
@@ -576,27 +566,19 @@
     float*  WvTf = ws + OFF_WVTF;
     float*  cvec = ws + OFF_CVEC;
     float*  U    = ws + OFF_U;
-    float*  W2   = ws + OFF_W2;
     float*  Hb   = ws + OFF_HB;
-    float*  Y    = ws + OFF_Y;
     float*  R    = ws + OFF_R;
     float*  OffV = ws + OFF_OFFV;
     ushort* Gbf  = (ushort*)(ws + OFF_GBF);
     ushort* WqT  = (ushort*)(ws + OFF_WQT);
     ushort* WkT  = (ushort*)(ws + OFF_WKT);
     ushort* Wvb  = (ushort*)(ws + OFF_WVB);
-    ushort* ZT   = (ushort*)(ws + OFF_ZT);
-    ushort* FT   = (ushort*)(ws + OFF_FT);
     ushort* Tbf  = (ushort*)(ws + OFF_TBF);
-
-    gram_mfma<<<dim3(8, 8, 3), 256, 0, stream>>>(x, Pg, Sp, Ghat);
-    reduce_mirror<<<385, 256, 0, stream>>>(Pg, Sp, Gbf, Ghat, S, Xbar);
-    stats_quad<<<dim3(64, 3), 256, 0, stream>>>(Wq, Wk, Wv, Ghat, Xbar,
-                                                bq, gq, betaq, bk, gk, betak,
-                                                bv, gv, betav, Wp, cvec,
-                                                WqT, WkT, Wvb, WkTf, WvTf);
-    zmida<<<13, 256, 0, stream>>>(WkT, WqT, ZT, Wp, WkTf, WvTf, S, cvec, U, W2, Y, R);
-    bcF<<<40, 256, 0, stream>>>(Wp, Gbf, WvTf, W2, Y, U, cvec, Hb, OffV, ZT, FT);
-    gemm_T<<<dim3(2, 2, 8), 256, 0, stream>>>(Wvb, FT, Tbf, U, cvec, R, Hb);
-    out_mfma<<<dim3(64, 8), 256, 0, stream>>>(Tbf, x, OffV, (float*)d_out);
-}
+    unsigned* Cnt = (unsigned*)(ws + OFF_CNT);
+
+    hipMemsetAsync((void*)Cnt, 0, 64, stream);
+    mono<<<256, 256, 0, stream>>>(x, Wq, bq, gq, betaq, Wk, bk, gk, betak,
+                                  Wv, bv, gv, betav, (float*)d_out,
+                                  Pg, Sp, S, Ghat, Xbar, Wp, WkTf, WvTf, cvec,
+                                  U, Hb, R, OffV, Gbf, WqT, WkT, Wvb, Tbf, Cnt);
+}
```

Result: slower. 318.2 us (+60.9%).
